# Kernel optimization log

Measured on AMD Instinct MI355X. Metric: run time of the kernel, lower is better.

Reference implementation:

```python
import jax, jax.numpy as jnp
import numpy as np

B, S, D, H, G, K = 4, 4096, 1024, 16, 4, 3
DG = D // G   # group channels = 256
DH = D // H   # head channels = 64


def setup_inputs() -> dict:
    key = jax.random.key(0)
    ks = jax.random.split(key, 8)
    def w(k, shape, std=0.02):
        return jax.random.normal(k, shape, jnp.float32) * std
    return {
        "x": jax.random.normal(ks[0], (B, S, D), jnp.float32),
        "Wq": w(ks[1], (D, D)), "bq": jnp.zeros((D,), jnp.float32),
        "Wk": w(ks[2], (D, D)), "bk": jnp.zeros((D,), jnp.float32),
        "Wv": w(ks[3], (D, D)), "bv": jnp.zeros((D,), jnp.float32),
        "Wo": w(ks[4], (D, D)), "bo": jnp.zeros((D,), jnp.float32),
        "Woff1": w(ks[5], (DG, DG, K)), "boff1": jnp.zeros((DG,), jnp.float32),
        "Woff2": w(ks[6], (DG,)),
        "bias_table": w(ks[7], (1, 1, S)),
    }


def reference(x, Wq, bq, Wk, bk, Wv, bv, Wo, bo, Woff1, boff1, Woff2, bias_table):
    bsz, seq, d = x.shape
    scale = d ** (-0.5)
    xc = jnp.transpose(x, (0, 2, 1))  # [B, D, S]

    # 1x1 conv projections == channel GEMMs
    q = jnp.einsum('oc,bcs->bos', Wq, xc) + bq[None, :, None]  # [B, D, S]

    # group: [B*G, DG, S]
    gq = q.reshape(bsz * G, DG, seq)
    # offset head: conv1d(k=3, pad=1) -> conv1d(k=1, no bias) -> [B*G, S]
    h = jax.lax.conv_general_dilated(
        gq, Woff1, window_strides=(1,), padding=((K // 2, K // 2),),
        dimension_numbers=('NCH', 'OIH', 'NCH')) + boff1[None, :, None]
    offset = jnp.einsum('c,bcs->bs', Woff2, h)
    offset = jnp.tanh(offset) * K  # offset_range_factor = kernel

    gx = xc.reshape(bsz * G, DG, seq)  # grouped x

    # faithful replication of _grid_sample_1d: F.grid_sample on feats [N,C,S,1]
    # with grid (x = vgrid_scaled -> width dim of size 1, y = 0 -> height dim of
    # size S), bilinear, zero padding, align_corners=False.
    grid = jnp.arange(seq, dtype=x.dtype)[None, :]
    vgrid_scaled = 2.0 * (grid + offset) / max(seq - 1, 1) - 1.0  # [B*G, S]
    ix = vgrid_scaled / 2.0                 # unnormalized width coord (W=1)
    wx = jnp.clip(1.0 - jnp.abs(ix), 0.0, 1.0)  # bilinear weight on width idx 0
    iy = (seq - 1) / 2.0                    # unnormalized height coord for y=0
    y0 = int(np.floor(iy)); y1 = min(y0 + 1, seq - 1)
    wy1 = float(iy - y0); wy0 = 1.0 - wy1
    feat_c = wy0 * gx[:, :, y0] + wy1 * gx[:, :, y1]  # [B*G, DG]
    x_sampled = feat_c[:, :, None] * wx[:, None, :]   # [B*G, DG, S]
    xs = x_sampled.reshape(bsz, d, seq)               # ungroup -> [B, D, S]

    k = jnp.einsum('oc,bcs->bos', Wk, xs) + bk[None, :, None]
    v = jnp.einsum('oc,bcs->bos', Wv, xs) + bv[None, :, None]

    qh = q.reshape(bsz * H, DH, seq)
    kh = k.reshape(bsz * H, DH, seq)
    vh = v.reshape(bsz * H, DH, seq) + bias_table[:, :, :seq]

    # channel attention: contract over sequence dim (as in the original einsum)
    scores = jnp.einsum('bis,bjs->bij', qh, kh) * scale  # [B*H, DH, DH]
    attn = jax.nn.softmax(scores, axis=-1)
    out = jnp.einsum('bij,bjs->bis', attn, vh)           # [B*H, DH, S]
    out = out.reshape(bsz, d, seq).transpose(0, 2, 1)     # [B, S, D]
    return jnp.einsum('bsd,od->bso', out, Wo) + bo
```

## Files before the change

kernel.cpp:

```cpp
#include <hip/hip_runtime.h>
#include <math.h>

#define BB 4
#define SS 4096
#define DD 1024
#define HH 16
#define GG 4
#define KK 3
#define DG 256
#define DH 64
#define CH 16
#define NCH (SS / CH)

enum : size_t {
  OFF_WEFF  = 0,
  OFF_OFFC  = 1024,
  OFF_WEQ   = 1280,
  OFF_ZT    = 13568,
  OFF_WX    = 210176,
  OFF_XWP   = 275712,
  OFF_XW    = 5518592,
  OFF_XS    = 5534976,
  OFF_SW    = 5539072,
  OFF_FEAT  = 5539328,
  OFF_KF    = 5543424,
  OFF_VF    = 5559808,
  OFF_AV    = 5576192,
  OFF_AB    = 5592576,
  OFF_C2    = 5596672,
  OFF_WAV   = 5600768,
  OFF_WOSUM = 5617152,
  WS_FLOATS = 5618176
};

__device__ __forceinline__ float wred_sum(float v) {
#pragma unroll
  for (int o = 32; o > 0; o >>= 1) v += __shfl_xor(v, o, 64);
  return v;
}
__device__ __forceinline__ float wred_max(float v) {
#pragma unroll
  for (int o = 32; o > 0; o >>= 1) v = fmaxf(v, __shfl_xor(v, o, 64));
  return v;
}

__global__ void k_pre1(const float* __restrict__ Woff1, const float* __restrict__ Woff2,
                       const float* __restrict__ x, const float* __restrict__ Wo,
                       float* __restrict__ ws) {
  const int t = threadIdx.x;
  const int lane = t & 63;
  if (blockIdx.x < 192) {
    const int widx = (blockIdx.x * 256 + t) >> 6;
    const int i = widx / 3, kk = widx - 3 * i;
    float a = 0.f;
#pragma unroll
    for (int u = 0; u < 4; ++u) {
      const int cc = lane + 64 * u;
      a += Woff2[cc] * Woff1[(size_t)(cc * DG + i) * KK + kk];
    }
    a = wred_sum(a);
    if (lane == 0) ws[OFF_WEFF + widx] = a;
  } else if (blockIdx.x < 208) {
    const int gid = (blockIdx.x - 192) * 256 + t;
    const int b = gid >> 10, c = gid & 1023;
    ws[OFF_FEAT + gid] = 0.5f * (x[((size_t)b * SS + 2047) * DD + c] +
                                 x[((size_t)b * SS + 2048) * DD + c]);
  } else {
    const int o = ((blockIdx.x - 208) * 256 + t) >> 6;
    const float4* wo = (const float4*)(Wo + (size_t)o * DD);
    float v = 0.f;
#pragma unroll
    for (int it = 0; it < 4; ++it) {
      const float4 a = wo[lane + 64 * it];
      v += a.x + a.y + a.z + a.w;
    }
    v = wred_sum(v);
    if (lane == 0) ws[OFF_WOSUM + o] = v;
  }
}

__global__ void k_pre2(const float* __restrict__ Wq, const float* __restrict__ bq,
                       const float* __restrict__ Woff2, const float* __restrict__ boff1,
                       const float* __restrict__ Wk, const float* __restrict__ Wv,
                       float* __restrict__ ws) {
  const float* Weff = ws + OFF_WEFF;
  const int t = threadIdx.x;
  const int lane = t & 63;
  if (blockIdx.x < 192) {
    const int j = blockIdx.x >> 4;
    const int c0 = (blockIdx.x & 15) * 64;
    const int g = j / 3, kk = j - 3 * g;
    const int q = t >> 6;
    float a = 0.f;
#pragma unroll 4
    for (int ii = 0; ii < 64; ++ii) {
      const int i = q * 64 + ii;
      a += Weff[i * KK + kk] * Wq[(size_t)(g * DG + i) * DD + c0 + lane];
    }
    __shared__ float red[4][64];
    red[q][lane] = a;
    __syncthreads();
    if (q == 0) {
      const float v = red[0][lane] + red[1][lane] + red[2][lane] + red[3][lane];
      ws[OFF_WEQ + (size_t)j * DD + c0 + lane] = v;
    }
  } else if (blockIdx.x == 192) {
    if (t >= 64) return;
    float beff = 0.f;
#pragma unroll
    for (int u = 0; u < 4; ++u) {
      const int cc = lane + 64 * u;
      beff += Woff2[cc] * boff1[cc];
    }
    beff = wred_sum(beff);
#pragma unroll
    for (int g = 0; g < 4; ++g) {
      float a = 0.f;
#pragma unroll
      for (int u = 0; u < 4; ++u) {
        const int i = lane + 64 * u;
        a += (Weff[i * 3 + 0] + Weff[i * 3 + 1] + Weff[i * 3 + 2]) * bq[g * DG + i];
      }
      a = wred_sum(a);
      if (lane == 0) ws[OFF_OFFC + g] = a + beff;
    }
  } else {
    const int widx = (blockIdx.x - 193) * 4 + (t >> 6);
    const int g = widx >> 10, o = widx & 1023;
    const float4 ak = ((const float4*)(Wk + (size_t)o * DD + g * DG))[lane];
    const float4 avv = ((const float4*)(Wv + (size_t)o * DD + g * DG))[lane];
    float kk[4], vv[4];
#pragma unroll
    for (int b = 0; b < 4; ++b) {
      const float4 f = ((const float4*)(ws + OFF_FEAT + (size_t)b * DD + g * DG))[lane];
      kk[b] = ak.x * f.x + ak.y * f.y + ak.z * f.z + ak.w * f.w;
      vv[b] = avv.x * f.x + avv.y * f.y + avv.z * f.z + avv.w * f.w;
    }
#pragma unroll
    for (int b = 0; b < 4; ++b) { kk[b] = wred_sum(kk[b]); vv[b] = wred_sum(vv[b]); }
    if (lane == 0) {
#pragma unroll
      for (int b = 0; b < 4; ++b) {
        ws[OFF_KF + ((size_t)(b * GG + g)) * DD + o] = kk[b];
        ws[OFF_VF + ((size_t)(b * GG + g)) * DD + o] = vv[b];
      }
    }
  }
}

__global__ __launch_bounds__(256, 2) void k_z(const float* __restrict__ x,
                                              const float* __restrict__ weq,
                                              float* __restrict__ zt) {
  const int lane = threadIdx.x & 63;
  const int wave = (blockIdx.x * blockDim.x + threadIdx.x) >> 6;
  const int nwaves = (gridDim.x * blockDim.x) >> 6;
  float4 w[12][4];
#pragma unroll
  for (int j = 0; j < 12; ++j)
#pragma unroll
    for (int it = 0; it < 4; ++it)
      w[j][it] = *(const float4*)(weq + (size_t)j * DD + 4 * (lane + 64 * it));
  for (int row = wave; row < BB * SS; row += nwaves) {
    const float4* xr = (const float4*)(x + (size_t)row * DD);
    float4 xv[4];
#pragma unroll
    for (int it = 0; it < 4; ++it) xv[it] = xr[lane + 64 * it];
    float acc[12];
#pragma unroll
    for (int j = 0; j < 12; ++j) {
      float a = 0.f;
#pragma unroll
      for (int it = 0; it < 4; ++it)
        a += xv[it].x * w[j][it].x + xv[it].y * w[j][it].y +
             xv[it].z * w[j][it].z + xv[it].w * w[j][it].w;
      acc[j] = a;
    }
#pragma unroll
    for (int j = 0; j < 12; ++j) acc[j] = wred_sum(acc[j]);
    if (lane == 0) {
#pragma unroll
      for (int j = 0; j < 12; ++j) zt[(size_t)row * 12 + j] = acc[j];
    }
  }
}

__global__ __launch_bounds__(256) void k_xw(const float* __restrict__ x,
                                            float* __restrict__ ws) {
  const int b = blockIdx.x >> 8;
  const int chunk = blockIdx.x & 255;
  const int s0 = chunk * CH;
  const int t = threadIdx.x;
  __shared__ float wxs[4][CH];

  if (t < 64) {
    const int g = t >> 4, si = t & 15;
    const int s = s0 + si;
    const size_t row = (size_t)b * SS + s;
    const float* zt = ws + OFF_ZT;
    float off = ws[OFF_OFFC + g];
    if (s > 0)      off += zt[(row - 1) * 12 + g * 3 + 0];
    off += zt[row * 12 + g * 3 + 1];
    if (s < SS - 1) off += zt[(row + 1) * 12 + g * 3 + 2];
    off = tanhf(off) * (float)KK;
    const float vg = 2.0f * ((float)s + off) / (float)(SS - 1) - 1.0f;
    float wvv = 1.0f - fabsf(0.5f * vg);
    wvv = fminf(fmaxf(wvv, 0.0f), 1.0f);
    wxs[g][si] = wvv;
    ws[OFF_WX + (size_t)(b * GG + g) * SS + s] = wvv;
  }
  __syncthreads();

  float4 aw[5] = {};
#pragma unroll 4
  for (int si = 0; si < CH; ++si) {
    const int s = s0 + si;
    const float4 f = *(const float4*)(x + (size_t)(b * SS + s) * DD + 4 * t);
    const float w0 = wxs[0][si], w1 = wxs[1][si], w2 = wxs[2][si], w3 = wxs[3][si];
    aw[0].x += f.x * w0; aw[0].y += f.y * w0; aw[0].z += f.z * w0; aw[0].w += f.w * w0;
    aw[1].x += f.x * w1; aw[1].y += f.y * w1; aw[1].z += f.z * w1; aw[1].w += f.w * w1;
    aw[2].x += f.x * w2; aw[2].y += f.y * w2; aw[2].z += f.z * w2; aw[2].w += f.w * w2;
    aw[3].x += f.x * w3; aw[3].y += f.y * w3; aw[3].z += f.z * w3; aw[3].w += f.w * w3;
    aw[4].x += f.x; aw[4].y += f.y; aw[4].z += f.z; aw[4].w += f.w;
  }
#pragma unroll
  for (int slot = 0; slot < 5; ++slot)
    *(float4*)(ws + OFF_XWP + (((size_t)(b * 5 + slot) * NCH + chunk) * DD) + 4 * t) = aw[slot];
}

__global__ void k_red(float* __restrict__ ws) {
  const int t = threadIdx.x;
  const int lane = t & 63;
  const int wvid = t >> 6;
  __shared__ float red[4][64];
  if (blockIdx.x < 320) {
    const int rb = blockIdx.x / 80;
    const int rem = blockIdx.x - rb * 80;
    const int slot = rem >> 4;
    const int c = (rem & 15) * 64 + lane;
    const float* base = ws + OFF_XWP + (size_t)(rb * 5 + slot) * NCH * DD;
    float a = 0.f;
#pragma unroll 8
    for (int ii = 0; ii < 64; ++ii)
      a += base[(size_t)(wvid * 64 + ii) * DD + c];
    red[wvid][lane] = a;
    __syncthreads();
    if (wvid == 0) {
      const float v = red[0][lane] + red[1][lane] + red[2][lane] + red[3][lane];
      if (slot < 4) ws[OFF_XW + ((size_t)(rb * GG + slot)) * DD + c] = v;
      else          ws[OFF_XS + (size_t)rb * DD + c] = v;
    }
  } else {
    const int w = blockIdx.x - 320;
    const float* wx = ws + OFF_WX + (size_t)w * SS;
    float a = 0.f;
#pragma unroll 4
    for (int it = 0; it < 16; ++it) a += wx[t + 256 * it];
    a = wred_sum(a);
    if (lane == 0) red[0][wvid] = a;
    __syncthreads();
    if (t == 0) ws[OFF_SW + w] = red[0][0] + red[0][1] + red[0][2] + red[0][3];
  }
}

__global__ void k_mid(const float* __restrict__ Wq, const float* __restrict__ bq,
                      const float* __restrict__ bk, const float* __restrict__ bv,
                      float* __restrict__ ws) {
  const int t = threadIdx.x;
  const int lane = t & 63;
  const int wave = blockIdx.x * 4 + (t >> 6);
  const int ab_ = wave >> 10, I = wave & 1023;
  const float4* wq = (const float4*)(Wq + (size_t)I * DD);
  float4 a[4];
#pragma unroll
  for (int it = 0; it < 4; ++it) a[it] = wq[lane + 64 * it];
  float acc[5] = {0.f, 0.f, 0.f, 0.f, 0.f};
#pragma unroll
  for (int g = 0; g < 4; ++g) {
    const float4* xw = (const float4*)(ws + OFF_XW + (size_t)(ab_ * GG + g) * DD);
#pragma unroll
    for (int it = 0; it < 4; ++it) {
      const float4 c = xw[lane + 64 * it];
      acc[g] += a[it].x * c.x + a[it].y * c.y + a[it].z * c.z + a[it].w * c.w;
    }
  }
  const float4* xs = (const float4*)(ws + OFF_XS + (size_t)ab_ * DD);
#pragma unroll
  for (int it = 0; it < 4; ++it) {
    const float4 c = xs[lane + 64 * it];
    acc[4] += a[it].x * c.x + a[it].y * c.y + a[it].z * c.z + a[it].w * c.w;
  }
#pragma unroll
  for (int u = 0; u < 5; ++u) acc[u] = wred_sum(acc[u]);
  const float bqi = bq[I];
  const float q0 = acc[0] + bqi * ws[OFF_SW + ab_ * GG + 0];
  const float q1 = acc[1] + bqi * ws[OFF_SW + ab_ * GG + 1];
  const float q2 = acc[2] + bqi * ws[OFF_SW + ab_ * GG + 2];
  const float q3 = acc[3] + bqi * ws[OFF_SW + ab_ * GG + 3];
  const float qs = acc[4] + (float)SS * bqi;
  const int J = (I & ~63) | lane;
  const float* Kf = ws + OFF_KF + (size_t)ab_ * GG * DD;
  float sc = q0 * Kf[0 * DD + J] + q1 * Kf[1 * DD + J] +
             q2 * Kf[2 * DD + J] + q3 * Kf[3 * DD + J] + bk[J] * qs;
  sc *= 0.03125f;
  const float m = wred_max(sc);
  const float e = expf(sc - m);
  const float sum = wred_sum(e);
  const float attn = e / sum;
  const float* Vf = ws + OFF_VF + (size_t)ab_ * GG * DD;
#pragma unroll
  for (int g = 0; g < 4; ++g) {
    const float av = wred_sum(attn * Vf[(size_t)g * DD + J]);
    if (lane == 0) ws[OFF_AV + (size_t)wave * 4 + g] = av;
  }
  const float abv = wred_sum(attn * bv[J]);
  if (lane == 0) ws[OFF_AB + wave] = abv;
}

__global__ void k_wav(const float* __restrict__ Wo, const float* __restrict__ bo,
                      float* __restrict__ ws) {
  const int gid = blockIdx.x * blockDim.x + threadIdx.x;
  const int lane = gid & 63;
  const int w = gid >> 6;
  if (w >= BB * DD) return;
  const int b = w >> 10, o = w & 1023;
  float acc0 = 0, acc1 = 0, acc2 = 0, acc3 = 0, acc4 = 0;
  const float4* wo4 = (const float4*)(Wo + (size_t)o * DD);
  const float* AV = ws + OFF_AV + (size_t)b * DD * 4;
  const float* Ab = ws + OFF_AB + (size_t)b * DD;
#pragma unroll
  for (int it = 0; it < 4; ++it) {
    const int d4 = lane + 64 * it;
    const float4 wv = wo4[d4];
    const float4 a0 = *(const float4*)(AV + (size_t)(4 * d4 + 0) * 4);
    const float4 a1 = *(const float4*)(AV + (size_t)(4 * d4 + 1) * 4);
    const float4 a2 = *(const float4*)(AV + (size_t)(4 * d4 + 2) * 4);
    const float4 a3 = *(const float4*)(AV + (size_t)(4 * d4 + 3) * 4);
    acc0 += wv.x * a0.x + wv.y * a1.x + wv.z * a2.x + wv.w * a3.x;
    acc1 += wv.x * a0.y + wv.y * a1.y + wv.z * a2.y + wv.w * a3.y;
    acc2 += wv.x * a0.z + wv.y * a1.z + wv.z * a2.z + wv.w * a3.z;
    acc3 += wv.x * a0.w + wv.y * a1.w + wv.z * a2.w + wv.w * a3.w;
    const float4 abv = *(const float4*)(Ab + 4 * d4);
    acc4 += wv.x * abv.x + wv.y * abv.y + wv.z * abv.z + wv.w * abv.w;
  }
  acc0 = wred_sum(acc0); acc1 = wred_sum(acc1); acc2 = wred_sum(acc2);
  acc3 = wred_sum(acc3); acc4 = wred_sum(acc4);
  if (lane == 0) {
    float* WAV = ws + OFF_WAV + (size_t)w * 4;
    WAV[0] = acc0; WAV[1] = acc1; WAV[2] = acc2; WAV[3] = acc3;
    ws[OFF_C2 + w] = acc4 + bo[o];
  }
}

__global__ __launch_bounds__(256) void k_out(const float* __restrict__ btab,
                                             const float* __restrict__ ws,
                                             float* __restrict__ out) {
  const int b = blockIdx.x >> 8;
  const int ch = blockIdx.x & 255;
  const int t = threadIdx.x;
  const int o0 = 4 * t;
  float4 wav[4];
#pragma unroll
  for (int io = 0; io < 4; ++io)
    wav[io] = *(const float4*)(ws + OFF_WAV + (size_t)(b * DD + o0 + io) * 4);
  const float4 c24 = *(const float4*)(ws + OFF_C2 + (size_t)b * DD + o0);
  const float4 wos4 = *(const float4*)(ws + OFF_WOSUM + o0);
  const float* wx = ws + OFF_WX;
  const int s0 = ch * CH;
#pragma unroll 2
  for (int si = 0; si < CH; ++si) {
    const int s = s0 + si;
    const float w0 = wx[(size_t)(b * GG + 0) * SS + s];
    const float w1 = wx[(size_t)(b * GG + 1) * SS + s];
    const float w2 = wx[(size_t)(b * GG + 2) * SS + s];
    const float w3 = wx[(size_t)(b * GG + 3) * SS + s];
    const float bt = btab[s];
    float4 val;
    val.x = c24.x + bt * wos4.x + w0 * wav[0].x + w1 * wav[0].y + w2 * wav[0].z + w3 * wav[0].w;
    val.y = c24.y + bt * wos4.y + w0 * wav[1].x + w1 * wav[1].y + w2 * wav[1].z + w3 * wav[1].w;
    val.z = c24.z + bt * wos4.z + w0 * wav[2].x + w1 * wav[2].y + w2 * wav[2].z + w3 * wav[2].w;
    val.w = c24.w + bt * wos4.w + w0 * wav[3].x + w1 * wav[3].y + w2 * wav[3].z + w3 * wav[3].w;
    *(float4*)(out + (size_t)(b * SS + s) * DD + o0) = val;
  }
}

extern "C" void kernel_launch(void* const* d_in, const int* in_sizes, int n_in,
                              void* d_out, int out_size, void* d_ws, size_t ws_size,
                              hipStream_t stream) {
  const float* x     = (const float*)d_in[0];
  const float* Wq    = (const float*)d_in[1];
  const float* bq    = (const float*)d_in[2];
  const float* Wk    = (const float*)d_in[3];
  const float* bk    = (const float*)d_in[4];
  const float* Wv    = (const float*)d_in[5];
  const float* bv    = (const float*)d_in[6];
  const float* Wo    = (const float*)d_in[7];
  const float* bo    = (const float*)d_in[8];
  const float* Woff1 = (const float*)d_in[9];
  const float* boff1 = (const float*)d_in[10];
  const float* Woff2 = (const float*)d_in[11];
  const float* btab  = (const float*)d_in[12];
  float* ws  = (float*)d_ws;
  float* out = (float*)d_out;

  k_pre1<<<464, 256, 0, stream>>>(Woff1, Woff2, x, Wo, ws);
  k_pre2<<<1217, 256, 0, stream>>>(Wq, bq, Woff2, boff1, Wk, Wv, ws);
  k_z<<<512, 256, 0, stream>>>(x, ws + OFF_WEQ, ws + OFF_ZT);
  k_xw<<<1024, 256, 0, stream>>>(x, ws);
  k_red<<<336, 256, 0, stream>>>(ws);
  k_mid<<<1024, 256, 0, stream>>>(Wq, bq, bk, bv, ws);
  k_wav<<<1024, 256, 0, stream>>>(Wo, bo, ws);
  k_out<<<1024, 256, 0, stream>>>(btab, ws, out);
}
```

Baseline: 213.1 us.

## Merge precompute kernels and fuse offset projection into weighted-sum kernel

Folds k_pre1 and k_pre2 into one precompute kernel, recomputing the effective offset weights per block instead of passing them through global memory. Fuses the 12-column offset projection (k_z) into the per-chunk x-weighting kernel, computing it for the chunk plus a one-row halo in shared memory, so the intermediate zt buffer and one extra pass over x go away. The per-group weight sums are now accumulated with atomics instead of a separate reduction branch. In exchange, halo rows are computed twice, the precompute blocks do more serial work, and the SW accumulator depends on being zeroed in the earlier kernel.

```diff
diff --git a/kernel.cpp b/kernel.cpp
--- a/kernel.cpp
+++ b/kernel.cpp
@@ -44,29 +44,83 @@
   return v;
 }
 
-__global__ void k_pre1(const float* __restrict__ Woff1, const float* __restrict__ Woff2,
-                       const float* __restrict__ x, const float* __restrict__ Wo,
-                       float* __restrict__ ws) {
+__global__ __launch_bounds__(256) void k_pre(
+    const float* __restrict__ x,  const float* __restrict__ Wq, const float* __restrict__ bq,
+    const float* __restrict__ Wk, const float* __restrict__ Wv, const float* __restrict__ Wo,
+    const float* __restrict__ Woff1, const float* __restrict__ boff1,
+    const float* __restrict__ Woff2, float* __restrict__ ws) {
   const int t = threadIdx.x;
   const int lane = t & 63;
-  if (blockIdx.x < 192) {
-    const int widx = (blockIdx.x * 256 + t) >> 6;
-    const int i = widx / 3, kk = widx - 3 * i;
-    float a = 0.f;
-#pragma unroll
-    for (int u = 0; u < 4; ++u) {
-      const int cc = lane + 64 * u;
-      a += Woff2[cc] * Woff1[(size_t)(cc * DG + i) * KK + kk];
-    }
-    a = wred_sum(a);
-    if (lane == 0) ws[OFF_WEFF + widx] = a;
-  } else if (blockIdx.x < 208) {
-    const int gid = (blockIdx.x - 192) * 256 + t;
-    const int b = gid >> 10, c = gid & 1023;
-    ws[OFF_FEAT + gid] = 0.5f * (x[((size_t)b * SS + 2047) * DD + c] +
-                                 x[((size_t)b * SS + 2048) * DD + c]);
+  const int wv = t >> 6;
+  const int bid = blockIdx.x;
+  __shared__ float smem[280];
+
+  if (bid < 12) {
+    const int j = bid, g = j / 3, kk = j - 3 * g;
+    float acc = 0.f;
+#pragma unroll 4
+    for (int cc = 0; cc < DG; ++cc)
+      acc += Woff2[cc] * Woff1[(size_t)(cc * DG + t) * KK + kk];
+    smem[t] = acc;
+    __syncthreads();
+    float a0 = 0.f, a1 = 0.f, a2 = 0.f, a3 = 0.f;
+    for (int i = 0; i < DG; ++i) {
+      const float wf = smem[i];
+      const float* wr = Wq + (size_t)(g * DG + i) * DD;
+      a0 += wf * wr[t];       a1 += wf * wr[t + 256];
+      a2 += wf * wr[t + 512]; a3 += wf * wr[t + 768];
+    }
+    float* wqd = ws + OFF_WEQ + (size_t)j * DD;
+    wqd[t] = a0; wqd[t + 256] = a1; wqd[t + 512] = a2; wqd[t + 768] = a3;
+  } else if (bid == 12) {
+    if (t < 16) ws[OFF_SW + t] = 0.f;
+    float accs = 0.f;
+#pragma unroll 4
+    for (int cc = 0; cc < DG; ++cc) {
+      const float* w1 = Woff1 + (size_t)(cc * DG + t) * KK;
+      accs += Woff2[cc] * (w1[0] + w1[1] + w1[2]);
+    }
+    float be = Woff2[t] * boff1[t];
+    be = wred_sum(be);
+    if (lane == 0) smem[256 + wv] = be;
+    __syncthreads();
+    const float beff = smem[256] + smem[257] + smem[258] + smem[259];
+#pragma unroll
+    for (int g = 0; g < 4; ++g) {
+      float a = accs * bq[g * DG + t];
+      a = wred_sum(a);
+      if (lane == 0) smem[260 + 4 * g + wv] = a;
+    }
+    __syncthreads();
+    if (t < 4)
+      ws[OFF_OFFC + t] = smem[260 + 4 * t] + smem[260 + 4 * t + 1] +
+                         smem[260 + 4 * t + 2] + smem[260 + 4 * t + 3] + beff;
+  } else if (bid < 1037) {
+    const int widx = (bid - 13) * 4 + wv;
+    const int g = widx >> 10, o = widx & 1023;
+    const float4 ak  = ((const float4*)(Wk + (size_t)o * DD + g * DG))[lane];
+    const float4 avv = ((const float4*)(Wv + (size_t)o * DD + g * DG))[lane];
+    float kk4[4], vv4[4];
+#pragma unroll
+    for (int b = 0; b < 4; ++b) {
+      const float4 xa = ((const float4*)(x + ((size_t)b * SS + 2047) * DD + g * DG))[lane];
+      const float4 xb = ((const float4*)(x + ((size_t)b * SS + 2048) * DD + g * DG))[lane];
+      const float fx = 0.5f * (xa.x + xb.x), fy = 0.5f * (xa.y + xb.y);
+      const float fz = 0.5f * (xa.z + xb.z), fw = 0.5f * (xa.w + xb.w);
+      kk4[b] = ak.x * fx + ak.y * fy + ak.z * fz + ak.w * fw;
+      vv4[b] = avv.x * fx + avv.y * fy + avv.z * fz + avv.w * fw;
+    }
+#pragma unroll
+    for (int b = 0; b < 4; ++b) { kk4[b] = wred_sum(kk4[b]); vv4[b] = wred_sum(vv4[b]); }
+    if (lane == 0) {
+#pragma unroll
+      for (int b = 0; b < 4; ++b) {
+        ws[OFF_KF + ((size_t)(b * GG + g)) * DD + o] = kk4[b];
+        ws[OFF_VF + ((size_t)(b * GG + g)) * DD + o] = vv4[b];
+      }
+    }
   } else {
-    const int o = ((blockIdx.x - 208) * 256 + t) >> 6;
+    const int o = (bid - 1037) * 4 + wv;
     const float4* wo = (const float4*)(Wo + (size_t)o * DD);
     float v = 0.f;
 #pragma unroll
@@ -79,143 +133,81 @@
   }
 }
 
-__global__ void k_pre2(const float* __restrict__ Wq, const float* __restrict__ bq,
-                       const float* __restrict__ Woff2, const float* __restrict__ boff1,
-                       const float* __restrict__ Wk, const float* __restrict__ Wv,
-                       float* __restrict__ ws) {
-  const float* Weff = ws + OFF_WEFF;
+__global__ __launch_bounds__(256, 2) void k_zxw(const float* __restrict__ x,
+                                                float* __restrict__ ws) {
   const int t = threadIdx.x;
   const int lane = t & 63;
-  if (blockIdx.x < 192) {
-    const int j = blockIdx.x >> 4;
-    const int c0 = (blockIdx.x & 15) * 64;
-    const int g = j / 3, kk = j - 3 * g;
-    const int q = t >> 6;
-    float a = 0.f;
-#pragma unroll 4
-    for (int ii = 0; ii < 64; ++ii) {
-      const int i = q * 64 + ii;
-      a += Weff[i * KK + kk] * Wq[(size_t)(g * DG + i) * DD + c0 + lane];
-    }
-    __shared__ float red[4][64];
-    red[q][lane] = a;
-    __syncthreads();
-    if (q == 0) {
-      const float v = red[0][lane] + red[1][lane] + red[2][lane] + red[3][lane];
-      ws[OFF_WEQ + (size_t)j * DD + c0 + lane] = v;
-    }
-  } else if (blockIdx.x == 192) {
-    if (t >= 64) return;
-    float beff = 0.f;
-#pragma unroll
-    for (int u = 0; u < 4; ++u) {
-      const int cc = lane + 64 * u;
-      beff += Woff2[cc] * boff1[cc];
-    }
-    beff = wred_sum(beff);
-#pragma unroll
-    for (int g = 0; g < 4; ++g) {
-      float a = 0.f;
-#pragma unroll
-      for (int u = 0; u < 4; ++u) {
-        const int i = lane + 64 * u;
-        a += (Weff[i * 3 + 0] + Weff[i * 3 + 1] + Weff[i * 3 + 2]) * bq[g * DG + i];
-      }
-      a = wred_sum(a);
-      if (lane == 0) ws[OFF_OFFC + g] = a + beff;
-    }
-  } else {
-    const int widx = (blockIdx.x - 193) * 4 + (t >> 6);
-    const int g = widx >> 10, o = widx & 1023;
-    const float4 ak = ((const float4*)(Wk + (size_t)o * DD + g * DG))[lane];
-    const float4 avv = ((const float4*)(Wv + (size_t)o * DD + g * DG))[lane];
-    float kk[4], vv[4];
-#pragma unroll
-    for (int b = 0; b < 4; ++b) {
-      const float4 f = ((const float4*)(ws + OFF_FEAT + (size_t)b * DD + g * DG))[lane];
-      kk[b] = ak.x * f.x + ak.y * f.y + ak.z * f.z + ak.w * f.w;
-      vv[b] = avv.x * f.x + avv.y * f.y + avv.z * f.z + avv.w * f.w;
-    }
-#pragma unroll
-    for (int b = 0; b < 4; ++b) { kk[b] = wred_sum(kk[b]); vv[b] = wred_sum(vv[b]); }
-    if (lane == 0) {
-#pragma unroll
-      for (int b = 0; b < 4; ++b) {
-        ws[OFF_KF + ((size_t)(b * GG + g)) * DD + o] = kk[b];
-        ws[OFF_VF + ((size_t)(b * GG + g)) * DD + o] = vv[b];
-      }
-    }
-  }
-}
-
-__global__ __launch_bounds__(256, 2) void k_z(const float* __restrict__ x,
-                                              const float* __restrict__ weq,
-                                              float* __restrict__ zt) {
-  const int lane = threadIdx.x & 63;
-  const int wave = (blockIdx.x * blockDim.x + threadIdx.x) >> 6;
-  const int nwaves = (gridDim.x * blockDim.x) >> 6;
-  float4 w[12][4];
-#pragma unroll
-  for (int j = 0; j < 12; ++j)
-#pragma unroll
-    for (int it = 0; it < 4; ++it)
-      w[j][it] = *(const float4*)(weq + (size_t)j * DD + 4 * (lane + 64 * it));
-  for (int row = wave; row < BB * SS; row += nwaves) {
-    const float4* xr = (const float4*)(x + (size_t)row * DD);
-    float4 xv[4];
-#pragma unroll
-    for (int it = 0; it < 4; ++it) xv[it] = xr[lane + 64 * it];
-    float acc[12];
-#pragma unroll
-    for (int j = 0; j < 12; ++j) {
-      float a = 0.f;
-#pragma unroll
-      for (int it = 0; it < 4; ++it)
-        a += xv[it].x * w[j][it].x + xv[it].y * w[j][it].y +
-             xv[it].z * w[j][it].z + xv[it].w * w[j][it].w;
-      acc[j] = a;
-    }
-#pragma unroll
-    for (int j = 0; j < 12; ++j) acc[j] = wred_sum(acc[j]);
-    if (lane == 0) {
-#pragma unroll
-      for (int j = 0; j < 12; ++j) zt[(size_t)row * 12 + j] = acc[j];
-    }
-  }
-}
-
-__global__ __launch_bounds__(256) void k_xw(const float* __restrict__ x,
-                                            float* __restrict__ ws) {
+  const int wv = t >> 6;
   const int b = blockIdx.x >> 8;
   const int chunk = blockIdx.x & 255;
   const int s0 = chunk * CH;
-  const int t = threadIdx.x;
-  __shared__ float wxs[4][CH];
+  __shared__ float zl[18][12];
+  __shared__ float wxs[64];
+
+  {
+    const float* weq = ws + OFF_WEQ;
+    float4 w[12][4];
+#pragma unroll
+    for (int j = 0; j < 12; ++j)
+#pragma unroll
+      for (int it = 0; it < 4; ++it)
+        w[j][it] = *(const float4*)(weq + (size_t)j * DD + 4 * (lane + 64 * it));
+    for (int r = wv; r < 18; r += 4) {
+      const int s = s0 - 1 + r;
+      if (s < 0 || s >= SS) continue;
+      const float4* xr = (const float4*)(x + ((size_t)b * SS + s) * DD);
+      float4 xv[4];
+#pragma unroll
+      for (int it = 0; it < 4; ++it) xv[it] = xr[lane + 64 * it];
+      float acc[12];
+#pragma unroll
+      for (int j = 0; j < 12; ++j) {
+        float a = 0.f;
+#pragma unroll
+        for (int it = 0; it < 4; ++it)
+          a += xv[it].x * w[j][it].x + xv[it].y * w[j][it].y +
+               xv[it].z * w[j][it].z + xv[it].w * w[j][it].w;
+        acc[j] = a;
+      }
+#pragma unroll
+      for (int j = 0; j < 12; ++j) acc[j] = wred_sum(acc[j]);
+      if (lane == 0) {
+#pragma unroll
+        for (int j = 0; j < 12; ++j) zl[r][j] = acc[j];
+      }
+    }
+  }
+  __syncthreads();
 
   if (t < 64) {
     const int g = t >> 4, si = t & 15;
     const int s = s0 + si;
-    const size_t row = (size_t)b * SS + s;
-    const float* zt = ws + OFF_ZT;
     float off = ws[OFF_OFFC + g];
-    if (s > 0)      off += zt[(row - 1) * 12 + g * 3 + 0];
-    off += zt[row * 12 + g * 3 + 1];
-    if (s < SS - 1) off += zt[(row + 1) * 12 + g * 3 + 2];
+    if (s > 0)      off += zl[si][g * 3 + 0];
+    off += zl[si + 1][g * 3 + 1];
+    if (s < SS - 1) off += zl[si + 2][g * 3 + 2];
     off = tanhf(off) * (float)KK;
     const float vg = 2.0f * ((float)s + off) / (float)(SS - 1) - 1.0f;
     float wvv = 1.0f - fabsf(0.5f * vg);
     wvv = fminf(fmaxf(wvv, 0.0f), 1.0f);
-    wxs[g][si] = wvv;
+    wxs[t] = wvv;
     ws[OFF_WX + (size_t)(b * GG + g) * SS + s] = wvv;
   }
   __syncthreads();
+
+  if (t < 4) {
+    float sl = 0.f;
+#pragma unroll
+    for (int si = 0; si < 16; ++si) sl += wxs[t * 16 + si];
+    atomicAdd(&ws[OFF_SW + b * GG + t], sl);
+  }
 
   float4 aw[5] = {};
 #pragma unroll 4
   for (int si = 0; si < CH; ++si) {
     const int s = s0 + si;
     const float4 f = *(const float4*)(x + (size_t)(b * SS + s) * DD + 4 * t);
-    const float w0 = wxs[0][si], w1 = wxs[1][si], w2 = wxs[2][si], w3 = wxs[3][si];
+    const float w0 = wxs[si], w1 = wxs[16 + si], w2 = wxs[32 + si], w3 = wxs[48 + si];
     aw[0].x += f.x * w0; aw[0].y += f.y * w0; aw[0].z += f.z * w0; aw[0].w += f.w * w0;
     aw[1].x += f.x * w1; aw[1].y += f.y * w1; aw[1].z += f.z * w1; aw[1].w += f.w * w1;
     aw[2].x += f.x * w2; aw[2].y += f.y * w2; aw[2].z += f.z * w2; aw[2].w += f.w * w2;
@@ -232,33 +224,21 @@
   const int lane = t & 63;
   const int wvid = t >> 6;
   __shared__ float red[4][64];
-  if (blockIdx.x < 320) {
-    const int rb = blockIdx.x / 80;
-    const int rem = blockIdx.x - rb * 80;
-    const int slot = rem >> 4;
-    const int c = (rem & 15) * 64 + lane;
-    const float* base = ws + OFF_XWP + (size_t)(rb * 5 + slot) * NCH * DD;
-    float a = 0.f;
+  const int rb = blockIdx.x / 80;
+  const int rem = blockIdx.x - rb * 80;
+  const int slot = rem >> 4;
+  const int c = (rem & 15) * 64 + lane;
+  const float* base = ws + OFF_XWP + (size_t)(rb * 5 + slot) * NCH * DD;
+  float a = 0.f;
 #pragma unroll 8
-    for (int ii = 0; ii < 64; ++ii)
-      a += base[(size_t)(wvid * 64 + ii) * DD + c];
-    red[wvid][lane] = a;
-    __syncthreads();
-    if (wvid == 0) {
-      const float v = red[0][lane] + red[1][lane] + red[2][lane] + red[3][lane];
-      if (slot < 4) ws[OFF_XW + ((size_t)(rb * GG + slot)) * DD + c] = v;
-      else          ws[OFF_XS + (size_t)rb * DD + c] = v;
-    }
-  } else {
-    const int w = blockIdx.x - 320;
-    const float* wx = ws + OFF_WX + (size_t)w * SS;
-    float a = 0.f;
-#pragma unroll 4
-    for (int it = 0; it < 16; ++it) a += wx[t + 256 * it];
-    a = wred_sum(a);
-    if (lane == 0) red[0][wvid] = a;
-    __syncthreads();
-    if (t == 0) ws[OFF_SW + w] = red[0][0] + red[0][1] + red[0][2] + red[0][3];
+  for (int ii = 0; ii < 64; ++ii)
+    a += base[(size_t)(wvid * 64 + ii) * DD + c];
+  red[wvid][lane] = a;
+  __syncthreads();
+  if (wvid == 0) {
+    const float v = red[0][lane] + red[1][lane] + red[2][lane] + red[3][lane];
+    if (slot < 4) ws[OFF_XW + ((size_t)(rb * GG + slot)) * DD + c] = v;
+    else          ws[OFF_XS + (size_t)rb * DD + c] = v;
   }
 }
 
@@ -330,17 +310,17 @@
 #pragma unroll
   for (int it = 0; it < 4; ++it) {
     const int d4 = lane + 64 * it;
-    const float4 wv = wo4[d4];
+    const float4 wv4 = wo4[d4];
     const float4 a0 = *(const float4*)(AV + (size_t)(4 * d4 + 0) * 4);
     const float4 a1 = *(const float4*)(AV + (size_t)(4 * d4 + 1) * 4);
     const float4 a2 = *(const float4*)(AV + (size_t)(4 * d4 + 2) * 4);
     const float4 a3 = *(const float4*)(AV + (size_t)(4 * d4 + 3) * 4);
-    acc0 += wv.x * a0.x + wv.y * a1.x + wv.z * a2.x + wv.w * a3.x;
-    acc1 += wv.x * a0.y + wv.y * a1.y + wv.z * a2.y + wv.w * a3.y;
-    acc2 += wv.x * a0.z + wv.y * a1.z + wv.z * a2.z + wv.w * a3.z;
-    acc3 += wv.x * a0.w + wv.y * a1.w + wv.z * a2.w + wv.w * a3.w;
+    acc0 += wv4.x * a0.x + wv4.y * a1.x + wv4.z * a2.x + wv4.w * a3.x;
+    acc1 += wv4.x * a0.y + wv4.y * a1.y + wv4.z * a2.y + wv4.w * a3.y;
+    acc2 += wv4.x * a0.z + wv4.y * a1.z + wv4.z * a2.z + wv4.w * a3.z;
+    acc3 += wv4.x * a0.w + wv4.y * a1.w + wv4.z * a2.w + wv4.w * a3.w;
     const float4 abv = *(const float4*)(Ab + 4 * d4);
-    acc4 += wv.x * abv.x + wv.y * abv.y + wv.z * abv.z + wv.w * abv.w;
+    acc4 += wv4.x * abv.x + wv4.y * abv.y + wv4.z * abv.z + wv4.w * abv.w;
   }
   acc0 = wred_sum(acc0); acc1 = wred_sum(acc1); acc2 = wred_sum(acc2);
   acc3 = wred_sum(acc3); acc4 = wred_sum(acc4);
@@ -362,7 +342,7 @@
 #pragma unroll
   for (int io = 0; io < 4; ++io)
     wav[io] = *(const float4*)(ws + OFF_WAV + (size_t)(b * DD + o0 + io) * 4);
-  const float4 c24 = *(const float4*)(ws + OFF_C2 + (size_t)b * DD + o0);
+  const float4 c24  = *(const float4*)(ws + OFF_C2 + (size_t)b * DD + o0);
   const float4 wos4 = *(const float4*)(ws + OFF_WOSUM + o0);
   const float* wx = ws + OFF_WX;
   const int s0 = ch * CH;
@@ -402,11 +382,9 @@
   float* ws  = (float*)d_ws;
   float* out = (float*)d_out;
 
-  k_pre1<<<464, 256, 0, stream>>>(Woff1, Woff2, x, Wo, ws);
-  k_pre2<<<1217, 256, 0, stream>>>(Wq, bq, Woff2, boff1, Wk, Wv, ws);
-  k_z<<<512, 256, 0, stream>>>(x, ws + OFF_WEQ, ws + OFF_ZT);
-  k_xw<<<1024, 256, 0, stream>>>(x, ws);
-  k_red<<<336, 256, 0, stream>>>(ws);
+  k_pre<<<1293, 256, 0, stream>>>(x, Wq, bq, Wk, Wv, Wo, Woff1, boff1, Woff2, ws);
+  k_zxw<<<1024, 256, 0, stream>>>(x, ws);
+  k_red<<<320, 256, 0, stream>>>(ws);
   k_mid<<<1024, 256, 0, stream>>>(Wq, bq, bk, bv, ws);
   k_wav<<<1024, 256, 0, stream>>>(Wo, bo, ws);
   k_out<<<1024, 256, 0, stream>>>(btab, ws, out);
```

New measurement: 257.9 us. +21.0%, slower.
